# Optimization experiments

Measured on AMD Instinct MI355X. Metric: run time of the kernel, lower is better.

## Reference

```python
import jax, jax.numpy as jnp
import numpy as np

ALPHA = 0.2  # LeakyReLU negative slope


def setup_inputs() -> dict:
    key = jax.random.key(0)
    k1, k2, k3 = jax.random.split(key, 3)
    B, N, F_in, F_out = 8, 2048, 256, 128
    h = jax.random.normal(k1, (B, N, F_in), dtype=jnp.float32)
    # nn.Linear(in, out, bias=False) weight applied as h @ W (stored [in, out])
    W = jax.random.normal(k2, (F_in, F_out), dtype=jnp.float32) * (1.0 / np.sqrt(F_in))
    # attention vector a: Linear(2*F_out, 1) -> vector of length 2*F_out
    a = jax.random.normal(k3, (2 * F_out,), dtype=jnp.float32) * (1.0 / np.sqrt(2 * F_out))
    return {"h": h, "W": W, "a": a}


def reference(h, W, a):
    # Wh: [B, N, F_out]
    Wh = jnp.einsum("bni,io->bno", h, W)
    F_out = W.shape[1]
    a1, a2 = a[:F_out], a[F_out:]
    # a(cat(Wh_i, Wh_j)) == Wh_i @ a1 + Wh_j @ a2 -- identical math, no O(N^2*2F) concat
    s1 = Wh @ a1  # [B, N] (source/row term)
    s2 = Wh @ a2  # [B, N] (target/col term)
    e = jax.nn.leaky_relu(s1[:, :, None] + s2[:, None, :], negative_slope=ALPHA)  # [B, N, N]
    attention = jax.nn.softmax(e, axis=-1)
    # dropout on attention is identity in eval mode (deterministic baseline)
    h_prime = jnp.einsum("bij,bjf->bif", attention, Wh)  # [B, N, F_out]
    return jax.nn.elu(h_prime)
```

## Files before the change

### kernel.cpp

```cpp
#include <hip/hip_runtime.h>
#include <math.h>
#include <stdint.h>

#define B_    8
#define N_    2048
#define FIN   256
#define FO    128
#define ALPHA 0.2f
#define NCHUNK 32
#define CHUNK  64

static const size_t OFF_WH    = 0;
static const size_t OFF_S1P   = OFF_WH    + (size_t)B_*N_*FO;
static const size_t OFF_S2P   = OFF_S1P   + (size_t)2*B_*N_;
static const size_t OFF_SSORT = OFF_S2P   + (size_t)2*B_*N_;
static const size_t OFF_SORD  = OFF_SSORT + (size_t)B_*N_;
static const size_t OFF_E2P   = OFF_SORD  + (size_t)B_*N_;
static const size_t OFF_E2N   = OFF_E2P   + (size_t)B_*N_;
static const size_t OFF_DPN   = OFF_E2N   + (size_t)B_*N_;
static const size_t OFF_KCUT  = OFF_DPN   + (size_t)2*B_*N_;
static const size_t OFF_SPN   = OFF_KCUT  + (size_t)B_*N_;

__global__ __launch_bounds__(256) void k1_gemm(const float* __restrict__ h,
                                               const float* __restrict__ W,
                                               const float* __restrict__ a,
                                               float* __restrict__ Wh,
                                               float* __restrict__ s1p,
                                               float* __restrict__ s2p) {
    __shared__ __align__(16) float hS[32][68];
    __shared__ __align__(16) float wS[32][64];
    __shared__ float red[2][64][20];

    const int tid  = threadIdx.x;
    const int mblk = blockIdx.x >> 1, nh = blockIdx.x & 1;
    const int row0 = mblk * 64, col0 = nh * 64;
    const int tn = tid & 15;
    const int tm = tid >> 4;
    const int h_r = tid >> 2, h_c0 = (tid & 3) * 8;

    float acc[4][4];
#pragma unroll
    for (int m = 0; m < 4; ++m)
#pragma unroll
        for (int c = 0; c < 4; ++c) acc[m][c] = 0.f;

    float4 ha, hb, wreg[2];
    ha = *(const float4*)&h[(size_t)(row0 + h_r) * FIN + h_c0];
    hb = *(const float4*)&h[(size_t)(row0 + h_r) * FIN + h_c0 + 4];
#pragma unroll
    for (int p = 0; p < 2; ++p) {
        int idx = p * 256 + tid, kW = idx >> 4, n4 = (idx & 15) * 4;
        wreg[p] = *(const float4*)&W[(size_t)kW * FO + col0 + n4];
    }

    for (int kt = 0; kt < FIN; kt += 32) {
        hS[h_c0 + 0][h_r] = ha.x; hS[h_c0 + 1][h_r] = ha.y;
        hS[h_c0 + 2][h_r] = ha.z; hS[h_c0 + 3][h_r] = ha.w;
        hS[h_c0 + 4][h_r] = hb.x; hS[h_c0 + 5][h_r] = hb.y;
        hS[h_c0 + 6][h_r] = hb.z; hS[h_c0 + 7][h_r] = hb.w;
#pragma unroll
        for (int p = 0; p < 2; ++p) {
            int idx = p * 256 + tid, kW = idx >> 4, n4 = (idx & 15) * 4;
            *(float4*)&wS[kW][n4] = wreg[p];
        }
        __syncthreads();

        if (kt + 32 < FIN) {
            ha = *(const float4*)&h[(size_t)(row0 + h_r) * FIN + kt + 32 + h_c0];
            hb = *(const float4*)&h[(size_t)(row0 + h_r) * FIN + kt + 32 + h_c0 + 4];
#pragma unroll
            for (int p = 0; p < 2; ++p) {
                int idx = p * 256 + tid, kW = idx >> 4, n4 = (idx & 15) * 4;
                wreg[p] = *(const float4*)&W[(size_t)(kt + 32 + kW) * FO + col0 + n4];
            }
        }

#pragma unroll 8
        for (int kk = 0; kk < 32; ++kk) {
            float4 hv = *(float4*)&hS[kk][4 * tm];
            float4 wv = *(float4*)&wS[kk][4 * tn];
            float hm[4] = {hv.x, hv.y, hv.z, hv.w};
            float wn4[4] = {wv.x, wv.y, wv.z, wv.w};
#pragma unroll
            for (int m = 0; m < 4; ++m)
#pragma unroll
                for (int c = 0; c < 4; ++c)
                    acc[m][c] += hm[m] * wn4[c];
        }
        __syncthreads();
    }

#pragma unroll
    for (int m = 0; m < 4; ++m) {
        float4 o = make_float4(acc[m][0], acc[m][1], acc[m][2], acc[m][3]);
        *(float4*)&Wh[(size_t)(row0 + 4 * tm + m) * FO + col0 + 4 * tn] = o;
    }

    float a1v[4], a2v[4];
#pragma unroll
    for (int c = 0; c < 4; ++c) {
        a1v[c] = a[col0 + 4 * tn + c];
        a2v[c] = a[FO + col0 + 4 * tn + c];
    }
#pragma unroll
    for (int m = 0; m < 4; ++m) {
        float p1 = 0.f, p2 = 0.f;
#pragma unroll
        for (int c = 0; c < 4; ++c) {
            p1 += acc[m][c] * a1v[c];
            p2 += acc[m][c] * a2v[c];
        }
        red[0][4 * tm + m][tn] = p1;
        red[1][4 * tm + m][tn] = p2;
    }
    __syncthreads();
    if (tid < 128) {
        int arr = tid >> 6, li = tid & 63;
        float s = 0.f;
#pragma unroll
        for (int g = 0; g < 16; ++g) s += red[arr][li][g];
        (arr ? s2p : s1p)[(size_t)nh * B_ * N_ + row0 + li] = s;
    }
}

__global__ __launch_bounds__(512) void k2a_rank(const float* __restrict__ s2p,
                                                float* __restrict__ ssort,
                                                int* __restrict__ sord,
                                                float* __restrict__ e2p,
                                                float* __restrict__ e2n) {
    __shared__ uint64_t keys[N_];
    __shared__ int part[512];
    const int b = blockIdx.x >> 5, c = blockIdx.x & 31;
    const int tid = threadIdx.x;

    for (int t = tid; t < N_; t += 512) {
        float s2v = s2p[b * N_ + t] + s2p[(size_t)B_ * N_ + b * N_ + t];
        unsigned u = __float_as_uint(s2v);
        u = (u & 0x80000000u) ? ~u : (u | 0x80000000u);
        keys[t] = ((uint64_t)u << 16) | (unsigned)t;
    }
    __syncthreads();

    const int le = tid & 63;
    const int e  = c * 64 + le;
    const int q  = tid >> 6;
    const uint64_t myk = keys[e];
    const uint64_t* kp = keys + q * 256;
    int cnt = 0;
#pragma unroll 8
    for (int kk = 0; kk < 256; ++kk) cnt += (int)(kp[kk] > myk);
    part[tid] = cnt;
    __syncthreads();

    if (tid < 64) {
        int rank = 0;
#pragma unroll
        for (int g = 0; g < 8; ++g) rank += part[tid + 64 * g];
        int ee = c * 64 + tid;
        float v = s2p[b * N_ + ee] + s2p[(size_t)B_ * N_ + b * N_ + ee];
        ssort[b * N_ + rank] = v;
        sord[b * N_ + rank]  = ee;
        e2p[b * N_ + rank] = expf(v);
        e2n[b * N_ + rank] = expf(ALPHA * v);
    }
}

__global__ __launch_bounds__(512) void kx_scan(const float* __restrict__ Wh,
                                               const int* __restrict__ sord,
                                               const float* __restrict__ e2p,
                                               const float* __restrict__ e2n,
                                               const float* __restrict__ ssort,
                                               const float* __restrict__ s1p,
                                               float2* __restrict__ SPN,
                                               float2* __restrict__ DPN,
                                               int* __restrict__ kcut) {
    __shared__ float2 qt[4][FO];
    __shared__ float sv[N_];
    __shared__ float2 wsum[8];
    const int tid = threadIdx.x;
    const int bid = blockIdx.x;

    if (bid < 256) {
        const int b = bid >> 5, ch = bid & 31;
        const int f = tid & 127, q = tid >> 7;
        const size_t base = (size_t)b * N_;
        const int ks = ch * CHUNK + q * 16;

        int ords[16]; float wp[16], wn[16], xv[16];
#pragma unroll
        for (int j = 0; j < 16; ++j) ords[j] = sord[base + ks + j];
#pragma unroll
        for (int j = 0; j < 16; ++j) { wp[j] = e2p[base + ks + j]; wn[j] = e2n[base + ks + j]; }
#pragma unroll
        for (int j = 0; j < 16; ++j) xv[j] = Wh[(base + ords[j]) * FO + f];

        float2 s[16];
        float ap = 0.f, an = 0.f;
#pragma unroll
        for (int j = 0; j < 16; ++j) {
            ap += wp[j] * xv[j];
            an += wn[j] * xv[j];
            s[j] = make_float2(ap, an);
        }
        qt[q][f] = make_float2(ap, an);
        __syncthreads();

        float op = 0.f, on = 0.f;
#pragma unroll
        for (int q2 = 0; q2 < 3; ++q2)
            if (q2 < q) { op += qt[q2][f].x; on += qt[q2][f].y; }

#pragma unroll
        for (int j = 0; j < 16; ++j)
            SPN[(base + ks + j) * FO + f] = make_float2(s[j].x + op, s[j].y + on);
    } else {
        const int b = bid - 256;
        const size_t base = (size_t)b * N_;

        float v[4], pv[4], nv[4], lp[4], ln[4];
        *(float4*)&v[0]  = *(const float4*)&ssort[base + tid * 4];
        *(float4*)&pv[0] = *(const float4*)&e2p[base + tid * 4];
        *(float4*)&nv[0] = *(const float4*)&e2n[base + tid * 4];
        float ap = 0.f, an = 0.f;
#pragma unroll
        for (int j = 0; j < 4; ++j) {
            sv[tid * 4 + j] = v[j];
            ap += pv[j]; lp[j] = ap;
            an += nv[j]; ln[j] = an;
        }

        float ip = ap, in2 = an;
        const int lane = tid & 63;
#pragma unroll
        for (int off = 1; off < 64; off <<= 1) {
            float tpv = __shfl_up(ip, off);
            float tnv = __shfl_up(in2, off);
            if (lane >= off) { ip += tpv; in2 += tnv; }
        }
        if (lane == 63) wsum[tid >> 6] = make_float2(ip, in2);
        __syncthreads();

        float basP = ip - ap, basN = in2 - an;
        const int w = tid >> 6;
#pragma unroll
        for (int w2 = 0; w2 < 7; ++w2)
            if (w2 < w) { basP += wsum[w2].x; basN += wsum[w2].y; }
#pragma unroll
        for (int j = 0; j < 4; ++j)
            DPN[base + tid * 4 + j] = make_float2(lp[j] + basP, ln[j] + basN);

        float tgt[4];
        int lo[4], hi[4];
#pragma unroll
        for (int r = 0; r < 4; ++r) {
            int row = tid + 512 * r;
            tgt[r] = -(s1p[base + row] + s1p[(size_t)B_ * N_ + base + row]);
            lo[r] = 0; hi[r] = N_;
        }
#pragma unroll
        for (int step = 0; step < 11; ++step) {
#pragma unroll
            for (int r = 0; r < 4; ++r) {
                int mid = (lo[r] + hi[r]) >> 1;
                bool live = lo[r] < hi[r];
                float pv2 = sv[mid & (N_ - 1)];
                bool cc = live && (pv2 >= tgt[r]);
                lo[r] = cc ? mid + 1 : lo[r];
                hi[r] = (live && !cc) ? mid : hi[r];
            }
        }
#pragma unroll
        for (int r = 0; r < 4; ++r) kcut[base + tid + 512 * r] = lo[r];
    }
}

__global__ __launch_bounds__(512) void k4_final(const float* __restrict__ s1p,
                                                const int* __restrict__ kcut,
                                                const float2* __restrict__ DPN,
                                                const float2* __restrict__ SPN,
                                                float* __restrict__ out) {
    __shared__ float2 ct[NCHUNK][FO];
    __shared__ float2 qTot[4][FO];
    __shared__ float sntN_lds[FO];
    __shared__ float2 s1e_lds[32];
    __shared__ float2 dpn_lds[32];
    __shared__ int    k_lds[32];

    const int bid = blockIdx.x;
    const int b   = bid >> 6;
    const int r0  = (bid & 63) * 32;
    const int tid = threadIdx.x;
    const int f = tid & 127, rr = tid >> 7;
    const size_t base = (size_t)b * N_;

    for (int idx = tid; idx < NCHUNK * FO; idx += 512) {
        int c = idx >> 7, ff = idx & 127;
        ct[c][ff] = SPN[(base + c * CHUNK + CHUNK - 1) * FO + ff];
    }
    if (tid < 32) {
        int row = r0 + tid;
        int k = kcut[base + row];
        k_lds[tid] = k;
        float s1v = s1p[base + row] + s1p[(size_t)B_ * N_ + base + row];
        s1e_lds[tid] = make_float2(expf(s1v), expf(ALPHA * s1v));
        dpn_lds[tid] = (k > 0) ? DPN[base + k - 1] : make_float2(0.f, 0.f);
    }
    __syncthreads();

    float rp = 0.f, rn = 0.f;
    for (int c = rr * 8; c < rr * 8 + 8; ++c) {
        float2 t = ct[c][f];
        ct[c][f] = make_float2(rp, rn);
        rp += t.x; rn += t.y;
    }
    qTot[rr][f] = make_float2(rp, rn);
    __syncthreads();
    float addP = 0.f, addN = 0.f;
#pragma unroll
    for (int q2 = 0; q2 < 3; ++q2)
        if (q2 < rr) { addP += qTot[q2][f].x; addN += qTot[q2][f].y; }
    if (rr > 0) {
        for (int c = rr * 8; c < rr * 8 + 8; ++c) {
            float2 t = ct[c][f];
            ct[c][f] = make_float2(t.x + addP, t.y + addN);
        }
    }
    if (tid < FO)
        sntN_lds[tid] = qTot[0][tid].y + qTot[1][tid].y + qTot[2][tid].y + qTot[3][tid].y;
    __syncthreads();

    const float dnt = DPN[base + N_ - 1].y;
    const float sntN = sntN_lds[f];

#pragma unroll 2
    for (int it = 0; it < 8; ++it) {
        const int lr   = it * 4 + rr;
        const int row  = r0 + lr;
        const float2 e1 = s1e_lds[lr];
        const float2 d  = dpn_lds[lr];
        const int k = k_lds[lr];

        float sp = 0.f, sn = 0.f;
        if (k > 0) {
            const int km1 = k - 1;
            const int c32 = km1 >> 6;
            float2 o  = ct[c32][f];
            float2 sl = SPN[(base + km1) * FO + f];
            sp = o.x + sl.x;
            sn = o.y + sl.y;
        }
        const float den = e1.x * d.x + e1.y * (dnt - d.y);
        const float num = e1.x * sp + e1.y * (sntN - sn);
        const float o = num / den;
        out[((size_t)b * N_ + row) * FO + f] = (o > 0.f) ? o : (expf(o) - 1.f);
    }
}

extern "C" void kernel_launch(void* const* d_in, const int* in_sizes, int n_in,
                              void* d_out, int out_size, void* d_ws, size_t ws_size,
                              hipStream_t stream) {
    const float* h = (const float*)d_in[0];
    const float* W = (const float*)d_in[1];
    const float* a = (const float*)d_in[2];
    float* out = (float*)d_out;
    float* ws = (float*)d_ws;

    float*  Wh    = ws + OFF_WH;
    float*  s1p   = ws + OFF_S1P;
    float*  s2p   = ws + OFF_S2P;
    float*  ssort = ws + OFF_SSORT;
    int*    sord  = (int*)(ws + OFF_SORD);
    float*  e2p   = ws + OFF_E2P;
    float*  e2n   = ws + OFF_E2N;
    float2* DPN   = (float2*)(ws + OFF_DPN);
    int*    kcut  = (int*)(ws + OFF_KCUT);
    float2* SPN   = (float2*)(ws + OFF_SPN);

    k1_gemm<<<dim3(512), dim3(256), 0, stream>>>(h, W, a, Wh, s1p, s2p);
    k2a_rank<<<dim3(B_ * 32), dim3(512), 0, stream>>>(s2p, ssort, sord, e2p, e2n);
    kx_scan<<<dim3(264), dim3(512), 0, stream>>>(Wh, sord, e2p, e2n, ssort, s1p,
                                                 SPN, DPN, kcut);
    k4_final<<<dim3(512), dim3(512), 0, stream>>>(s1p, kcut, DPN, SPN, out);
}
```

Before: 53.05 us.

## Compute projection GEMM with split-bf16 MFMA and 4-way partial attention scores

Replaces the FP32 FMA tiled GEMM for Wh with MFMA bf16 instructions, splitting each fp32 operand into hi/lo bf16 parts and using three products to keep close to fp32 accuracy. Each block now covers a full 64x128 output tile with 8 waves. The s1/s2 projections are reduced with wave shuffles, and partial sums are stored per column group, four of them now. All consumers are updated to add four partials instead of two. The goal is to cut the FMA-bound cost of the first kernel, at the price of conversion overhead and slightly reduced precision.

```diff
diff --git a/kernel.cpp b/kernel.cpp
--- a/kernel.cpp
+++ b/kernel.cpp
@@ -10,10 +10,15 @@
 #define NCHUNK 32
 #define CHUNK  64
 
+typedef __attribute__((ext_vector_type(8))) __bf16 bf16x8;
+typedef __attribute__((ext_vector_type(8))) short short8_t;
+typedef __attribute__((ext_vector_type(4))) short short4_t;
+typedef __attribute__((ext_vector_type(4))) float f32x4;
+
 static const size_t OFF_WH    = 0;
 static const size_t OFF_S1P   = OFF_WH    + (size_t)B_*N_*FO;
-static const size_t OFF_S2P   = OFF_S1P   + (size_t)2*B_*N_;
-static const size_t OFF_SSORT = OFF_S2P   + (size_t)2*B_*N_;
+static const size_t OFF_S2P   = OFF_S1P   + (size_t)4*B_*N_;
+static const size_t OFF_SSORT = OFF_S2P   + (size_t)4*B_*N_;
 static const size_t OFF_SORD  = OFF_SSORT + (size_t)B_*N_;
 static const size_t OFF_E2P   = OFF_SORD  + (size_t)B_*N_;
 static const size_t OFF_E2N   = OFF_E2P   + (size_t)B_*N_;
@@ -21,105 +26,142 @@
 static const size_t OFF_KCUT  = OFF_DPN   + (size_t)2*B_*N_;
 static const size_t OFF_SPN   = OFF_KCUT  + (size_t)B_*N_;
 
-__global__ __launch_bounds__(256) void k1_gemm(const float* __restrict__ h,
+__device__ __forceinline__ unsigned short bf16_rne(float x) {
+    unsigned u = __float_as_uint(x);
+    unsigned r = (u + 0x7FFFu + ((u >> 16) & 1u)) >> 16;
+    return (unsigned short)r;
+}
+
+__global__ __launch_bounds__(512) void k1_gemm(const float* __restrict__ h,
                                                const float* __restrict__ W,
                                                const float* __restrict__ a,
                                                float* __restrict__ Wh,
                                                float* __restrict__ s1p,
                                                float* __restrict__ s2p) {
-    __shared__ __align__(16) float hS[32][68];
-    __shared__ __align__(16) float wS[32][64];
-    __shared__ float red[2][64][20];
+    __shared__ short hS_hi[64][40], hS_lo[64][40];
+    __shared__ short wS_hi[128][40], wS_lo[128][40];
 
     const int tid  = threadIdx.x;
-    const int mblk = blockIdx.x >> 1, nh = blockIdx.x & 1;
-    const int row0 = mblk * 64, col0 = nh * 64;
-    const int tn = tid & 15;
-    const int tm = tid >> 4;
-    const int h_r = tid >> 2, h_c0 = (tid & 3) * 8;
-
-    float acc[4][4];
-#pragma unroll
-    for (int m = 0; m < 4; ++m)
-#pragma unroll
-        for (int c = 0; c < 4; ++c) acc[m][c] = 0.f;
-
-    float4 ha, hb, wreg[2];
-    ha = *(const float4*)&h[(size_t)(row0 + h_r) * FIN + h_c0];
-    hb = *(const float4*)&h[(size_t)(row0 + h_r) * FIN + h_c0 + 4];
-#pragma unroll
-    for (int p = 0; p < 2; ++p) {
-        int idx = p * 256 + tid, kW = idx >> 4, n4 = (idx & 15) * 4;
-        wreg[p] = *(const float4*)&W[(size_t)kW * FO + col0 + n4];
-    }
-
-    for (int kt = 0; kt < FIN; kt += 32) {
-        hS[h_c0 + 0][h_r] = ha.x; hS[h_c0 + 1][h_r] = ha.y;
-        hS[h_c0 + 2][h_r] = ha.z; hS[h_c0 + 3][h_r] = ha.w;
-        hS[h_c0 + 4][h_r] = hb.x; hS[h_c0 + 5][h_r] = hb.y;
-        hS[h_c0 + 6][h_r] = hb.z; hS[h_c0 + 7][h_r] = hb.w;
-#pragma unroll
-        for (int p = 0; p < 2; ++p) {
-            int idx = p * 256 + tid, kW = idx >> 4, n4 = (idx & 15) * 4;
-            *(float4*)&wS[kW][n4] = wreg[p];
+    const int lane = tid & 63, wv = tid >> 6;
+    const int mh = wv & 1, ng = wv >> 1;
+    const int l15 = lane & 15, l4 = lane >> 4;
+    const int row0 = blockIdx.x * 64;
+
+    const int h_r = tid >> 3, h_kq = (tid & 7) * 4;
+    const int w_c = tid & 127, w_kb = (tid >> 7) * 8;
+
+    f32x4 acc[2][2];
+#pragma unroll
+    for (int i = 0; i < 2; ++i)
+#pragma unroll
+        for (int j = 0; j < 2; ++j) acc[i][j] = (f32x4){0.f, 0.f, 0.f, 0.f};
+
+    float4 hv = *(const float4*)&h[(size_t)(row0 + h_r) * FIN + h_kq];
+    float wf[8];
+#pragma unroll
+    for (int s = 0; s < 8; ++s) wf[s] = W[(size_t)(w_kb + s) * FO + w_c];
+
+    for (int k0 = 0; k0 < FIN; k0 += 32) {
+        {
+            float hf[4] = {hv.x, hv.y, hv.z, hv.w};
+            short4_t hhi, hlo;
+#pragma unroll
+            for (int s = 0; s < 4; ++s) {
+                unsigned short hb = bf16_rne(hf[s]);
+                float hbf = __uint_as_float((unsigned)hb << 16);
+                hhi[s] = (short)hb;
+                hlo[s] = (short)bf16_rne(hf[s] - hbf);
+            }
+            *(short4_t*)&hS_hi[h_r][h_kq] = hhi;
+            *(short4_t*)&hS_lo[h_r][h_kq] = hlo;
+
+            short8_t whi, wlo;
+#pragma unroll
+            for (int s = 0; s < 8; ++s) {
+                unsigned short wb = bf16_rne(wf[s]);
+                float wbf = __uint_as_float((unsigned)wb << 16);
+                whi[s] = (short)wb;
+                wlo[s] = (short)bf16_rne(wf[s] - wbf);
+            }
+            *(short8_t*)&wS_hi[w_c][w_kb] = whi;
+            *(short8_t*)&wS_lo[w_c][w_kb] = wlo;
         }
         __syncthreads();
 
-        if (kt + 32 < FIN) {
-            ha = *(const float4*)&h[(size_t)(row0 + h_r) * FIN + kt + 32 + h_c0];
-            hb = *(const float4*)&h[(size_t)(row0 + h_r) * FIN + kt + 32 + h_c0 + 4];
-#pragma unroll
-            for (int p = 0; p < 2; ++p) {
-                int idx = p * 256 + tid, kW = idx >> 4, n4 = (idx & 15) * 4;
-                wreg[p] = *(const float4*)&W[(size_t)(kt + 32 + kW) * FO + col0 + n4];
-            }
-        }
-
-#pragma unroll 8
-        for (int kk = 0; kk < 32; ++kk) {
-            float4 hv = *(float4*)&hS[kk][4 * tm];
-            float4 wv = *(float4*)&wS[kk][4 * tn];
-            float hm[4] = {hv.x, hv.y, hv.z, hv.w};
-            float wn4[4] = {wv.x, wv.y, wv.z, wv.w};
-#pragma unroll
-            for (int m = 0; m < 4; ++m)
-#pragma unroll
-                for (int c = 0; c < 4; ++c)
-                    acc[m][c] += hm[m] * wn4[c];
-        }
+        if (k0 + 32 < FIN) {
+            hv = *(const float4*)&h[(size_t)(row0 + h_r) * FIN + k0 + 32 + h_kq];
+#pragma unroll
+            for (int s = 0; s < 8; ++s)
+                wf[s] = W[(size_t)(k0 + 32 + w_kb + s) * FO + w_c];
+        }
+
+        bf16x8 a_hi[2], a_lo[2], b_hi[2], b_lo[2];
+#pragma unroll
+        for (int i = 0; i < 2; ++i) {
+            int r = (mh * 2 + i) * 16 + l15;
+            a_hi[i] = __builtin_bit_cast(bf16x8, *(short8_t*)&hS_hi[r][l4 * 8]);
+            a_lo[i] = __builtin_bit_cast(bf16x8, *(short8_t*)&hS_lo[r][l4 * 8]);
+        }
+#pragma unroll
+        for (int j = 0; j < 2; ++j) {
+            int c = (ng * 2 + j) * 16 + l15;
+            b_hi[j] = __builtin_bit_cast(bf16x8, *(short8_t*)&wS_hi[c][l4 * 8]);
+            b_lo[j] = __builtin_bit_cast(bf16x8, *(short8_t*)&wS_lo[c][l4 * 8]);
+        }
+#pragma unroll
+        for (int i = 0; i < 2; ++i)
+#pragma unroll
+            for (int j = 0; j < 2; ++j) {
+                acc[i][j] = __builtin_amdgcn_mfma_f32_16x16x32_bf16(a_hi[i], b_hi[j], acc[i][j], 0, 0, 0);
+                acc[i][j] = __builtin_amdgcn_mfma_f32_16x16x32_bf16(a_hi[i], b_lo[j], acc[i][j], 0, 0, 0);
+                acc[i][j] = __builtin_amdgcn_mfma_f32_16x16x32_bf16(a_lo[i], b_hi[j], acc[i][j], 0, 0, 0);
+            }
         __syncthreads();
     }
 
 #pragma unroll
-    for (int m = 0; m < 4; ++m) {
-        float4 o = make_float4(acc[m][0], acc[m][1], acc[m][2], acc[m][3]);
-        *(float4*)&Wh[(size_t)(row0 + 4 * tm + m) * FO + col0 + 4 * tn] = o;
-    }
-
-    float a1v[4], a2v[4];
-#pragma unroll
-    for (int c = 0; c < 4; ++c) {
-        a1v[c] = a[col0 + 4 * tn + c];
-        a2v[c] = a[FO + col0 + 4 * tn + c];
-    }
-#pragma unroll
-    for (int m = 0; m < 4; ++m) {
-        float p1 = 0.f, p2 = 0.f;
-#pragma unroll
-        for (int c = 0; c < 4; ++c) {
-            p1 += acc[m][c] * a1v[c];
-            p2 += acc[m][c] * a2v[c];
-        }
-        red[0][4 * tm + m][tn] = p1;
-        red[1][4 * tm + m][tn] = p2;
-    }
-    __syncthreads();
-    if (tid < 128) {
-        int arr = tid >> 6, li = tid & 63;
-        float s = 0.f;
-#pragma unroll
-        for (int g = 0; g < 16; ++g) s += red[arr][li][g];
-        (arr ? s2p : s1p)[(size_t)nh * B_ * N_ + row0 + li] = s;
+    for (int i = 0; i < 2; ++i)
+#pragma unroll
+        for (int j = 0; j < 2; ++j) {
+            int colg = (ng * 2 + j) * 16 + l15;
+#pragma unroll
+            for (int reg = 0; reg < 4; ++reg) {
+                int rowg = row0 + (mh * 2 + i) * 16 + l4 * 4 + reg;
+                Wh[(size_t)rowg * FO + colg] = acc[i][j][reg];
+            }
+        }
+
+    float a1v[2], a2v[2];
+#pragma unroll
+    for (int j = 0; j < 2; ++j) {
+        int c = (ng * 2 + j) * 16 + l15;
+        a1v[j] = a[c];
+        a2v[j] = a[FO + c];
+    }
+#pragma unroll
+    for (int i = 0; i < 2; ++i) {
+        float p1[4], p2[4];
+#pragma unroll
+        for (int reg = 0; reg < 4; ++reg) {
+            p1[reg] = acc[i][0][reg] * a1v[0] + acc[i][1][reg] * a1v[1];
+            p2[reg] = acc[i][0][reg] * a2v[0] + acc[i][1][reg] * a2v[1];
+        }
+#pragma unroll
+        for (int m = 1; m < 16; m <<= 1) {
+#pragma unroll
+            for (int reg = 0; reg < 4; ++reg) {
+                p1[reg] += __shfl_xor(p1[reg], m);
+                p2[reg] += __shfl_xor(p2[reg], m);
+            }
+        }
+        if (l15 == 0) {
+#pragma unroll
+            for (int reg = 0; reg < 4; ++reg) {
+                int rowg = row0 + (mh * 2 + i) * 16 + l4 * 4 + reg;
+                s1p[(size_t)ng * (B_ * N_) + rowg] = p1[reg];
+                s2p[(size_t)ng * (B_ * N_) + rowg] = p2[reg];
+            }
+        }
     }
 }
 
@@ -132,9 +174,11 @@
     __shared__ int part[512];
     const int b = blockIdx.x >> 5, c = blockIdx.x & 31;
     const int tid = threadIdx.x;
+    const size_t SZ = (size_t)B_ * N_;
 
     for (int t = tid; t < N_; t += 512) {
-        float s2v = s2p[b * N_ + t] + s2p[(size_t)B_ * N_ + b * N_ + t];
+        size_t ix = (size_t)b * N_ + t;
+        float s2v = s2p[ix] + s2p[SZ + ix] + s2p[2 * SZ + ix] + s2p[3 * SZ + ix];
         unsigned u = __float_as_uint(s2v);
         u = (u & 0x80000000u) ? ~u : (u | 0x80000000u);
         keys[t] = ((uint64_t)u << 16) | (unsigned)t;
@@ -157,7 +201,8 @@
 #pragma unroll
         for (int g = 0; g < 8; ++g) rank += part[tid + 64 * g];
         int ee = c * 64 + tid;
-        float v = s2p[b * N_ + ee] + s2p[(size_t)B_ * N_ + b * N_ + ee];
+        size_t ix = (size_t)b * N_ + ee;
+        float v = s2p[ix] + s2p[SZ + ix] + s2p[2 * SZ + ix] + s2p[3 * SZ + ix];
         ssort[b * N_ + rank] = v;
         sord[b * N_ + rank]  = ee;
         e2p[b * N_ + rank] = expf(v);
@@ -179,6 +224,7 @@
     __shared__ float2 wsum[8];
     const int tid = threadIdx.x;
     const int bid = blockIdx.x;
+    const size_t SZ = (size_t)B_ * N_;
 
     if (bid < 256) {
         const int b = bid >> 5, ch = bid & 31;
@@ -253,8 +299,8 @@
         int lo[4], hi[4];
 #pragma unroll
         for (int r = 0; r < 4; ++r) {
-            int row = tid + 512 * r;
-            tgt[r] = -(s1p[base + row] + s1p[(size_t)B_ * N_ + base + row]);
+            size_t row = base + tid + 512 * r;
+            tgt[r] = -(s1p[row] + s1p[SZ + row] + s1p[2 * SZ + row] + s1p[3 * SZ + row]);
             lo[r] = 0; hi[r] = N_;
         }
 #pragma unroll
@@ -292,6 +338,7 @@
     const int tid = threadIdx.x;
     const int f = tid & 127, rr = tid >> 7;
     const size_t base = (size_t)b * N_;
+    const size_t SZ = (size_t)B_ * N_;
 
     for (int idx = tid; idx < NCHUNK * FO; idx += 512) {
         int c = idx >> 7, ff = idx & 127;
@@ -301,7 +348,8 @@
         int row = r0 + tid;
         int k = kcut[base + row];
         k_lds[tid] = k;
-        float s1v = s1p[base + row] + s1p[(size_t)B_ * N_ + base + row];
+        size_t rix = base + row;
+        float s1v = s1p[rix] + s1p[SZ + rix] + s1p[2 * SZ + rix] + s1p[3 * SZ + rix];
         s1e_lds[tid] = make_float2(expf(s1v), expf(ALPHA * s1v));
         dpn_lds[tid] = (k > 0) ? DPN[base + k - 1] : make_float2(0.f, 0.f);
     }
@@ -376,7 +424,7 @@
     int*    kcut  = (int*)(ws + OFF_KCUT);
     float2* SPN   = (float2*)(ws + OFF_SPN);
 
-    k1_gemm<<<dim3(512), dim3(256), 0, stream>>>(h, W, a, Wh, s1p, s2p);
+    k1_gemm<<<dim3(B_ * N_ / 64), dim3(512), 0, stream>>>(h, W, a, Wh, s1p, s2p);
     k2a_rank<<<dim3(B_ * 32), dim3(512), 0, stream>>>(s2p, ssort, sord, e2p, e2n);
     kx_scan<<<dim3(264), dim3(512), 0, stream>>>(Wh, sord, e2p, e2n, ssort, s1p,
                                                  SPN, DPN, kcut);
```

Result: faster. 45.35 us, median of 2 (-14.5%).
